# Optimization experiments

Hardware: AMD Instinct MI355X
Metric: run time of the kernel (lower is better)

## Reference

```python
import jax, jax.numpy as jnp
import numpy as np

N, E, D, ED, L = 40000, 640000, 128, 16, 3  # nodes, edges, emb_dim, edge_dim, num_layer
BN_EPS = 1e-5


def setup_inputs() -> dict:
    key = jax.random.key(0)
    ks = jax.random.split(key, 20)
    s = 0.05
    inp = {
        "x": jax.random.normal(ks[0], (N, D), jnp.float32),
        "edge_attr": jax.random.normal(ks[1], (E, ED), jnp.float32),
        # node encoder Linear(input_dim, emb_dim)
        "node_W": jax.random.normal(ks[2], (D, D), jnp.float32) * s,
        "node_b": jnp.zeros((D,), jnp.float32),
        # per-layer params (leading dim L)
        "edge_W": jax.random.normal(ks[3], (L, ED, D), jnp.float32) * s,
        "edge_b": jnp.zeros((L, D), jnp.float32),
        "attn_W": jax.random.normal(ks[4], (L, 2 * D, 1), jnp.float32) * s,
        "attn_b": jnp.zeros((L, 1), jnp.float32),
        "eps": jnp.zeros((L,), jnp.float32),
        "W1": jax.random.normal(ks[5], (L, D, 2 * D), jnp.float32) * s,
        "b1": jnp.zeros((L, 2 * D), jnp.float32),
        "bn1_g": jnp.ones((L, 2 * D), jnp.float32),
        "bn1_b": jnp.zeros((L, 2 * D), jnp.float32),
        "W2": jax.random.normal(ks[6], (L, 2 * D, D), jnp.float32) * s,
        "b2": jnp.zeros((L, D), jnp.float32),
        "bn_g": jnp.ones((L, D), jnp.float32),
        "bn_b": jnp.zeros((L, D), jnp.float32),
        "edge_index": jax.random.randint(ks[7], (2, E), 0, N, jnp.int32),
    }
    return inp


def _bn_eval(h, g, b):
    # BatchNorm1d in eval with running_mean=0, running_var=1
    return g * h * (1.0 / np.sqrt(1.0 + BN_EPS)) + b


def reference(x, edge_attr, node_W, node_b, edge_W, edge_b, attn_W, attn_b,
              eps, W1, b1, bn1_g, bn1_b, W2, b2, bn_g, bn_b, edge_index):
    src, dst = edge_index[0], edge_index[1]
    h = x @ node_W + node_b  # node_encoder, [N, D]
    for l in range(L):
        e = edge_attr @ edge_W[l] + edge_b[l]       # [E, D] edge embedding
        xj = h[src]                                  # [E, D] source gather
        xi = h[dst]                                  # [E, D] target gather
        a = jax.nn.sigmoid(jnp.concatenate([xi, xj], axis=-1) @ attn_W[l] + attn_b[l])  # [E,1]
        msg = jax.nn.relu(xj * a + e)                # fused per-edge message
        agg = jax.ops.segment_sum(msg, dst, num_segments=N)  # scatter-add aggregate
        z = (1.0 + eps[l]) * h + agg
        # GIN mlp: Linear -> BN(eval) -> ReLU -> Linear
        z = _bn_eval(z @ W1[l] + b1[l], bn1_g[l], bn1_b[l])
        z = jax.nn.relu(z)
        z = z @ W2[l] + b2[l]
        # outer BatchNorm(eval); dropout = identity in eval; JK='last', no residual
        z = _bn_eval(z, bn_g[l], bn_b[l])
        if l < L - 1:
            z = jax.nn.relu(z)
        h = z
    return h
```

## Files before the change

kernel.cpp:

```cpp
#include <hip/hip_runtime.h>
#include <math.h>

#define NN 40000
#define EE 640000
#define DD 128
#define EDD 16
#define LL 3
#define TEB 64

__device__ __constant__ float kBnInv = 0.9999950000374997f;

typedef __bf16 bf16x8 __attribute__((ext_vector_type(8)));
typedef float  f32x16 __attribute__((ext_vector_type(16)));
typedef float  f32x4  __attribute__((ext_vector_type(4)));
typedef float  f32x2  __attribute__((ext_vector_type(2)));

__device__ __forceinline__ unsigned pack_bf2(float a, float b) {
    unsigned ua = __float_as_uint(a), ub = __float_as_uint(b);
    ua = (ua + 0x7fffu + ((ua >> 16) & 1u)) >> 16;
    ub = (ub + 0x7fffu + ((ub >> 16) & 1u)) & 0xffff0000u;
    return ua | ub;
}
__device__ __forceinline__ unsigned short bf16r(float x) {
    unsigned u = __float_as_uint(x);
    u = (u + 0x7fffu + ((u >> 16) & 1u)) >> 16;
    return (unsigned short)u;
}

__global__ __launch_bounds__(256) void node_enc_kernel(
    const float* __restrict__ x, const float* __restrict__ W,
    const float* __restrict__ b,
    const float* __restrict__ aW, const float* __restrict__ eps_p,
    float* __restrict__ h, unsigned* __restrict__ hb,
    float* __restrict__ pi, float* __restrict__ pj, float* __restrict__ z)
{
    __shared__ float xs[32][DD];
    const int t = threadIdx.x;
    const long rowbase = (long)blockIdx.x * 32;

    const float4* x4 = (const float4*)(x + rowbase * DD);
    float4* xs4 = (float4*)&xs[0][0];
#pragma unroll
    for (int i = 0; i < 4; i++) xs4[t + i * 256] = x4[t + i * 256];
    __syncthreads();

    const int c  = (t & 31) * 4;
    const int r0 = (t >> 5) * 4;

    float acc[4][4] = {};
    for (int k4 = 0; k4 < DD; k4 += 4) {
        float4 xr[4];
#pragma unroll
        for (int i = 0; i < 4; i++) xr[i] = *(const float4*)&xs[r0 + i][k4];
#pragma unroll
        for (int kk = 0; kk < 4; kk++) {
            const float4 w = *(const float4*)(W + (k4 + kk) * DD + c);
#pragma unroll
            for (int i = 0; i < 4; i++) {
                const float xv = ((const float*)&xr[i])[kk];
                acc[i][0] = fmaf(xv, w.x, acc[i][0]);
                acc[i][1] = fmaf(xv, w.y, acc[i][1]);
                acc[i][2] = fmaf(xv, w.z, acc[i][2]);
                acc[i][3] = fmaf(xv, w.w, acc[i][3]);
            }
        }
    }
    const float4 bv  = *(const float4*)(b + c);
    const float4 awi = *(const float4*)(aW + c);
    const float4 awj = *(const float4*)(aW + DD + c);
    const float ep = 1.0f + eps_p[0];

    float pa[4], pb[4];
#pragma unroll
    for (int i = 0; i < 4; i++) {
        const long row = rowbase + r0 + i;
        float4 ov = { acc[i][0] + bv.x, acc[i][1] + bv.y,
                      acc[i][2] + bv.z, acc[i][3] + bv.w };
        *(float4*)(h + row * DD + c) = ov;
        uint2 pv = { pack_bf2(ov.x, ov.y), pack_bf2(ov.z, ov.w) };
        *(uint2*)(hb + row * 64 + (c >> 1)) = pv;
        float4 zv = { ep * ov.x, ep * ov.y, ep * ov.z, ep * ov.w };
        *(float4*)(z + row * DD + c) = zv;
        pa[i] = ov.x * awi.x + ov.y * awi.y + ov.z * awi.z + ov.w * awi.w;
        pb[i] = ov.x * awj.x + ov.y * awj.y + ov.z * awj.z + ov.w * awj.w;
    }
#pragma unroll
    for (int off = 1; off < 32; off <<= 1) {
#pragma unroll
        for (int i = 0; i < 4; i++) {
            pa[i] += __shfl_xor(pa[i], off, 64);
            pb[i] += __shfl_xor(pb[i], off, 64);
        }
    }
    if ((t & 31) == 0) {
#pragma unroll
        for (int i = 0; i < 4; i++) {
            pi[rowbase + r0 + i] = pa[i];
            pj[rowbase + r0 + i] = pb[i];
        }
    }
}

__global__ __launch_bounds__(256) void wcast_kernel(
    const float* __restrict__ W1, const float* __restrict__ W2,
    const float* __restrict__ eW,
    unsigned short* __restrict__ w1t, unsigned short* __restrict__ w2t,
    unsigned short* __restrict__ ewt)
{
    const int idx = blockIdx.x * 256 + threadIdx.x;
    const int l = idx >> 15, r = idx & 32767;
    {   const int n = r >> 7, k = r & 127;
        w1t[idx] = bf16r(W1[(l << 15) + (k << 8) + n]);
    }
    {   const int n = r >> 8, k = r & 255;
        w2t[idx] = bf16r(W2[(l << 15) + (k << 7) + n]);
    }
    if (idx < LL * 2048) {
        const int le = idx >> 11, re = idx & 2047;
        const int n = re >> 4, k = re & 15;
        ewt[idx] = bf16r(eW[(le << 11) + (k << 7) + n]);
    }
}

__global__ __launch_bounds__(256) void hist_kernel(
    const int* __restrict__ edge_index, int* __restrict__ counts)
{
    const int i = blockIdx.x * 256 + threadIdx.x;
    atomicAdd(&counts[edge_index[EE + i]], 1);
}

__global__ __launch_bounds__(256) void scan1_kernel(
    const int* __restrict__ counts, int* __restrict__ scanned,
    int* __restrict__ partials)
{
    __shared__ int sdata[256];
    const int t = threadIdx.x;
    const int base = blockIdx.x * 1024 + t * 4;
    int v[4]; int sum = 0;
#pragma unroll
    for (int i = 0; i < 4; i++) {
        const int idx = base + i;
        v[i] = (idx < NN) ? counts[idx] : 0;
        sum += v[i];
    }
    sdata[t] = sum;
    __syncthreads();
    for (int off = 1; off < 256; off <<= 1) {
        int x = (t >= off) ? sdata[t - off] : 0;
        __syncthreads();
        sdata[t] += x;
        __syncthreads();
    }
    int run = sdata[t] - sum;
#pragma unroll
    for (int i = 0; i < 4; i++) {
        const int idx = base + i;
        if (idx < NN) scanned[idx] = run;
        run += v[i];
    }
    if (t == 255) partials[blockIdx.x] = sdata[255];
}

__global__ void scan2_kernel(int* __restrict__ partials)
{
    if (threadIdx.x == 0) {
        int run = 0;
        for (int i = 0; i < 40; i++) { int v = partials[i]; partials[i] = run; run += v; }
    }
}

__global__ __launch_bounds__(256) void scan3_kernel(
    const int* __restrict__ scanned, const int* __restrict__ partials,
    int* __restrict__ offsets, int* __restrict__ cursor)
{
    const int idx = blockIdx.x * 256 + threadIdx.x;
    if (idx < NN) {
        const int off = scanned[idx] + partials[idx >> 10];
        offsets[idx] = off;
        cursor[idx]  = off;
    }
}

__global__ __launch_bounds__(256) void scatter_kernel(
    const int* __restrict__ edge_index, const float* __restrict__ edge_attr,
    int* __restrict__ cursor,
    int* __restrict__ srcs_p, int* __restrict__ dstd_p,
    unsigned* __restrict__ ea_b)
{
    const int i = blockIdx.x * 256 + threadIdx.x;
    const int src = edge_index[i];
    const int dst = edge_index[EE + i];
    const int pos = atomicAdd(&cursor[dst], 1);
    srcs_p[pos] = src << 6;
    dstd_p[pos] = dst << 7;

    const float4* sp = (const float4*)(edge_attr + (long)i * EDD);
    const float4 s0 = sp[0], s1 = sp[1], s2 = sp[2], s3 = sp[3];
    uint4 o0 = { pack_bf2(s0.x, s0.y), pack_bf2(s0.z, s0.w),
                 pack_bf2(s1.x, s1.y), pack_bf2(s1.z, s1.w) };
    uint4 o1 = { pack_bf2(s2.x, s2.y), pack_bf2(s2.z, s2.w),
                 pack_bf2(s3.x, s3.y), pack_bf2(s3.z, s3.w) };
    *(uint4*)(ea_b + (long)pos * 8)     = o0;
    *(uint4*)(ea_b + (long)pos * 8 + 4) = o1;
}

__global__ __launch_bounds__(256) void edge_msg_kernel(
    const unsigned* __restrict__ hb, const unsigned* __restrict__ ea_b,
    const float* __restrict__ pi, const float* __restrict__ pj,
    const int* __restrict__ srcs_p, const int* __restrict__ dstd_p,
    const float* __restrict__ ab_p,
    const unsigned short* __restrict__ eWt, const float* __restrict__ eb,
    float* __restrict__ z)
{
    __shared__ __align__(16) unsigned short sh_eb[TEB * DD];
    __shared__ int   sh_src[TEB];
    __shared__ int   sh_dst[TEB];
    __shared__ float sh_a[TEB];

    const int t = threadIdx.x;
    const int wid = t >> 6, lane = t & 63;
    const long e0 = (long)blockIdx.x * TEB;

    if (t < TEB) {
        const int ss = srcs_p[e0 + t];
        const int dd = dstd_p[e0 + t];
        sh_src[t] = ss;
        sh_dst[t] = dd;
        const float s = pi[dd >> 7] + pj[ss >> 6] + ab_p[0];
        sh_a[t] = 1.0f / (1.0f + expf(-s));
    }

    const int l31 = lane & 31, half = lane >> 5;
    const int mt = wid & 1, nt0 = wid >> 1;
    const bf16x8 afr  = *(const bf16x8*)(ea_b + (e0 + mt * 32 + l31) * 8 + half * 4);
    const bf16x8 bfr0 = *(const bf16x8*)(eWt + (nt0 * 32 + l31) * 16 + half * 8);
    const bf16x8 bfr1 = *(const bf16x8*)(eWt + ((nt0 + 2) * 32 + l31) * 16 + half * 8);

    __syncthreads();

    const int base = wid * 16;
    unsigned u[16];
#pragma unroll
    for (int j = 0; j < 16; j++)
        u[j] = hb[sh_src[base + j] + lane];

    {
        f32x16 a0 = {0.0f,0.0f,0.0f,0.0f, 0.0f,0.0f,0.0f,0.0f,
                     0.0f,0.0f,0.0f,0.0f, 0.0f,0.0f,0.0f,0.0f};
        f32x16 a1 = a0;
        a0 = __builtin_amdgcn_mfma_f32_32x32x16_bf16(afr, bfr0, a0, 0, 0, 0);
        a1 = __builtin_amdgcn_mfma_f32_32x32x16_bf16(afr, bfr1, a1, 0, 0, 0);
        const float eb0 = eb[nt0 * 32 + l31];
        const float eb1 = eb[(nt0 + 2) * 32 + l31];
        const int rb = mt * 32 + 4 * half;
        const int cA = nt0 * 32 + l31;
        const int cB = (nt0 + 2) * 32 + l31;
#pragma unroll
        for (int r = 0; r < 16; r++) {
            const int row = rb + (r & 3) + 8 * (r >> 2);
            sh_eb[row * DD + cA] = bf16r(a0[r] + eb0);
            sh_eb[row * DD + cB] = bf16r(a1[r] + eb1);
        }
    }
    __syncthreads();

    const int c0 = lane * 2;
    const f32x2 zero2 = { 0.0f, 0.0f };
    f32x2 acc = zero2;
    int cur = sh_dst[base];

#pragma unroll
    for (int j = 0; j < 16; j++) {
        const int dd = sh_dst[base + j];
        if (dd != cur) {
            atomicAdd(&z[cur + c0],     acc[0]);
            atomicAdd(&z[cur + c0 + 1], acc[1]);
            acc = zero2; cur = dd;
        }
        const float a = sh_a[base + j];
        const unsigned ue = *(const unsigned*)&sh_eb[(base + j) * DD + c0];
        const f32x2 ev = { __uint_as_float(ue << 16),
                           __uint_as_float(ue & 0xffff0000u) };
        const f32x2 xj = { __uint_as_float(u[j] << 16),
                           __uint_as_float(u[j] & 0xffff0000u) };
        const f32x2 av = { a, a };
        f32x2 m = __builtin_elementwise_fma(xj, av, ev);
        m = __builtin_elementwise_max(m, zero2);
        acc += m;
    }
    atomicAdd(&z[cur + c0],     acc[0]);
    atomicAdd(&z[cur + c0 + 1], acc[1]);
}

__global__ __launch_bounds__(256) void mlp_mfma_kernel(
    const float* __restrict__ zin,
    const unsigned short* __restrict__ w1t, const unsigned short* __restrict__ w2t,
    const float* __restrict__ b1, const float* __restrict__ g1, const float* __restrict__ bb1,
    const float* __restrict__ b2, const float* __restrict__ g2, const float* __restrict__ bb2,
    const float* __restrict__ aWn, const float* __restrict__ epsn_p,
    float* __restrict__ out, unsigned* __restrict__ hb,
    float* __restrict__ pi, float* __restrict__ pj, float* __restrict__ z,
    const int do_relu)
{
    __shared__ __align__(16) unsigned short zsb[64][136];
    __shared__ __align__(16) unsigned short usb[64][264];
    __shared__ float sh_pi[64], sh_pj[64];
    const int t = threadIdx.x;
    const int wid = t >> 6, lane = t & 63;
    const long rowbase = (long)blockIdx.x * 64;

    if (t < 64) { sh_pi[t] = 0.0f; sh_pj[t] = 0.0f; }

    {
        const float4* z4 = (const float4*)(zin + rowbase * DD);
#pragma unroll
        for (int i = 0; i < 8; i++) {
            const int idx = t + i * 256;
            const float4 v = z4[idx];
            const int row = idx >> 5;
            const int c4  = (idx & 31) * 4;
            uint2 pv = { pack_bf2(v.x, v.y), pack_bf2(v.z, v.w) };
            *(uint2*)&zsb[row][c4] = pv;
        }
    }
    __syncthreads();

    const int mrow  = lane & 15;
    const int quad  = lane >> 4;
    const f32x4 vzero = {0.0f, 0.0f, 0.0f, 0.0f};

    {
        const int nt0 = wid * 4;
        bf16x8 bf[4][4];
#pragma unroll
        for (int j = 0; j < 4; j++) {
            const unsigned short* wp = w1t + ((nt0 + j) * 16 + mrow) * 128 + quad * 8;
#pragma unroll
            for (int ks = 0; ks < 4; ks++)
                bf[j][ks] = *(const bf16x8*)(wp + ks * 32);
        }
        float gg[4], bi[4], bt[4];
#pragma unroll
        for (int j = 0; j < 4; j++) {
            const int c = (nt0 + j) * 16 + mrow;
            gg[j] = g1[c]; bi[j] = b1[c]; bt[j] = bb1[c];
        }
#pragma unroll
        for (int rt = 0; rt < 4; rt++) {
            bf16x8 af[4];
#pragma unroll
            for (int ks = 0; ks < 4; ks++)
                af[ks] = *(const bf16x8*)&zsb[rt * 16 + mrow][ks * 32 + quad * 8];
            f32x4 acc[4];
#pragma unroll
            for (int j = 0; j < 4; j++) acc[j] = vzero;
#pragma unroll
            for (int j = 0; j < 4; j++)
#pragma unroll
                for (int ks = 0; ks < 4; ks++)
                    acc[j] = __builtin_amdgcn_mfma_f32_16x16x32_bf16(af[ks], bf[j][ks], acc[j], 0, 0, 0);
#pragma unroll
            for (int j = 0; j < 4; j++) {
                const int c = (nt0 + j) * 16 + mrow;
#pragma unroll
                for (int r = 0; r < 4; r++) {
                    const int row = rt * 16 + quad * 4 + r;
                    const float u = fmaxf(fmaf(gg[j] * (acc[j][r] + bi[j]), kBnInv, bt[j]), 0.0f);
                    const float up = __shfl_xor(u, 1, 64);
                    if ((mrow & 1) == 0)
                        *(unsigned*)&usb[row][c] = pack_bf2(u, up);
                }
            }
        }
    }
    __syncthreads();

    {
        const int nt0 = wid * 2;
        bf16x8 bf[2][8];
#pragma unroll
        for (int j = 0; j < 2; j++) {
            const unsigned short* wp = w2t + ((nt0 + j) * 16 + mrow) * 256 + quad * 8;
#pragma unroll
            for (int ks = 0; ks < 8; ks++)
                bf[j][ks] = *(const bf16x8*)(wp + ks * 32);
        }
        float gg[2], bi[2], bt[2], awi[2], awj[2];
#pragma unroll
        for (int j = 0; j < 2; j++) {
            const int c = (nt0 + j) * 16 + mrow;
            gg[j] = g2[c]; bi[j] = b2[c]; bt[j] = bb2[c];
            awi[j] = aWn[c]; awj[j] = aWn[DD + c];
        }
        const float epn = do_relu ? (1.0f + epsn_p[0]) : 0.0f;

#pragma unroll
        for (int rt = 0; rt < 4; rt++) {
            bf16x8 af[8];
#pragma unroll
            for (int ks = 0; ks < 8; ks++)
                af[ks] = *(const bf16x8*)&usb[rt * 16 + mrow][ks * 32 + quad * 8];
            f32x4 acc[2];
            acc[0] = vzero; acc[1] = vzero;
#pragma unroll
            for (int j = 0; j < 2; j++)
#pragma unroll
                for (int ks = 0; ks < 8; ks++)
                    acc[j] = __builtin_amdgcn_mfma_f32_16x16x32_bf16(af[ks], bf[j][ks], acc[j], 0, 0, 0);

            float si[4] = {0, 0, 0, 0}, sj[4] = {0, 0, 0, 0};
#pragma unroll
            for (int j = 0; j < 2; j++) {
                const int c = (nt0 + j) * 16 + mrow;
#pragma unroll
                for (int r = 0; r < 4; r++) {
                    const long row = rowbase + rt * 16 + quad * 4 + r;
                    float v = fmaf(gg[j] * (acc[j][r] + bi[j]), kBnInv, bt[j]);
                    if (do_relu) {
                        v = fmaxf(v, 0.0f);
                        z[row * DD + c] = epn * v;
                        si[r] = fmaf(v, awi[j], si[r]);
                        sj[r] = fmaf(v, awj[j], sj[r]);
                    }
                    out[row * DD + c] = v;
                    const float vp = __shfl_xor(v, 1, 64);
                    if ((mrow & 1) == 0)
                        hb[row * 64 + (c >> 1)] = pack_bf2(v, vp);
                }
            }
            if (do_relu) {
#pragma unroll
                for (int off = 1; off < 16; off <<= 1) {
#pragma unroll
                    for (int r = 0; r < 4; r++) {
                        si[r] += __shfl_xor(si[r], off, 64);
                        sj[r] += __shfl_xor(sj[r], off, 64);
                    }
                }
                if (mrow == 0) {
#pragma unroll
                    for (int r = 0; r < 4; r++) {
                        atomicAdd(&sh_pi[rt * 16 + quad * 4 + r], si[r]);
                        atomicAdd(&sh_pj[rt * 16 + quad * 4 + r], sj[r]);
                    }
                }
            }
        }
    }
    if (do_relu) {
        __syncthreads();
        if (t < 64) {
            pi[rowbase + t] = sh_pi[t];
            pj[rowbase + t] = sh_pj[t];
        }
    }
}

extern "C" void kernel_launch(void* const* d_in, const int* in_sizes, int n_in,
                              void* d_out, int out_size, void* d_ws, size_t ws_size,
                              hipStream_t stream)
{
    const float* x         = (const float*)d_in[0];
    const float* edge_attr = (const float*)d_in[1];
    const float* node_W    = (const float*)d_in[2];
    const float* node_b    = (const float*)d_in[3];
    const float* edge_W    = (const float*)d_in[4];
    const float* edge_b    = (const float*)d_in[5];
    const float* attn_W    = (const float*)d_in[6];
    const float* attn_b    = (const float*)d_in[7];
    const float* eps       = (const float*)d_in[8];
    const float* W1        = (const float*)d_in[9];
    const float* b1        = (const float*)d_in[10];
    const float* bn1_g     = (const float*)d_in[11];
    const float* bn1_b     = (const float*)d_in[12];
    const float* W2        = (const float*)d_in[13];
    const float* b2        = (const float*)d_in[14];
    const float* bn_g      = (const float*)d_in[15];
    const float* bn_b      = (const float*)d_in[16];
    const int*   edge_index= (const int*)d_in[17];

    float* h    = (float*)d_ws;
    float* z    = h + (size_t)NN * DD;
    float* pi   = z + (size_t)NN * DD;
    float* pj   = pi + NN;
    unsigned* ea_b = (unsigned*)(pj + NN);
    unsigned* hbuf = ea_b + (size_t)EE * 8;
    unsigned short* w1t = (unsigned short*)(hbuf + (size_t)NN * 64);
    unsigned short* w2t = w1t + (size_t)LL * 32768;
    unsigned short* ewt = w2t + (size_t)LL * 32768;
    int* counts  = (int*)(ewt + (size_t)LL * 2048);
    int* offsets = counts + NN;
    int* cursor  = offsets + NN;
    int* scanned = cursor + NN;
    int* partials= scanned + 40960;
    int* srcs_p  = partials + 64;
    int* dstd_p  = srcs_p + EE;
    float* out = (float*)d_out;

    node_enc_kernel<<<NN / 32, 256, 0, stream>>>(
        x, node_W, node_b, attn_W, eps, h, hbuf, pi, pj, z);
    wcast_kernel<<<LL * 128, 256, 0, stream>>>(W1, W2, edge_W, w1t, w2t, ewt);

    hipMemsetAsync(counts, 0, NN * sizeof(int), stream);
    hist_kernel<<<EE / 256, 256, 0, stream>>>(edge_index, counts);
    scan1_kernel<<<40, 256, 0, stream>>>(counts, scanned, partials);
    scan2_kernel<<<1, 64, 0, stream>>>(partials);
    scan3_kernel<<<(NN + 255) / 256, 256, 0, stream>>>(scanned, partials, offsets, cursor);
    scatter_kernel<<<EE / 256, 256, 0, stream>>>(
        edge_index, edge_attr, cursor, srcs_p, dstd_p, ea_b);

    for (int l = 0; l < LL; l++) {
        const int ln = (l + 1 < LL) ? (l + 1) : l;
        edge_msg_kernel<<<EE / TEB, 256, 0, stream>>>(
            hbuf, ea_b, pi, pj, srcs_p, dstd_p, attn_b + l,
            ewt + (size_t)l * 2048, edge_b + (size_t)l * DD, z);
        mlp_mfma_kernel<<<NN / 64, 256, 0, stream>>>(
            z,
            w1t + (size_t)l * 32768, w2t + (size_t)l * 32768,
            b1 + (size_t)l * 2 * DD, bn1_g + (size_t)l * 2 * DD, bn1_b + (size_t)l * 2 * DD,
            b2 + (size_t)l * DD, bn_g + (size_t)l * DD, bn_b + (size_t)l * DD,
            attn_W + (size_t)ln * 2 * DD, eps + ln,
            (l == LL - 1) ? out : h, hbuf, pi, pj, z, (l < LL - 1) ? 1 : 0);
    }
}
```

Measured before the change: 531.2 us.

## Assign destination-node ranges to blocks and aggregate edge messages in LDS

The edge message kernel is re-partitioned so each block owns 32 consecutive destination nodes and walks their CSR-sorted edge range, accumulating messages in shared memory instead of issuing global float atomics. The block then writes z = (1+eps)*h + agg directly, so the node encoder and MLP kernels no longer pre-write z. This removes the global atomic traffic and the extra z stores. In exchange it adds load imbalance across blocks with uneven degree, extra syncthreads per 64-edge tile, and shared-memory atomics.

```diff
diff --git a/kernel.cpp b/kernel.cpp
--- a/kernel.cpp
+++ b/kernel.cpp
@@ -7,6 +7,7 @@
 #define EDD 16
 #define LL 3
 #define TEB 64
+#define NPB 32
 
 __device__ __constant__ float kBnInv = 0.9999950000374997f;
 
@@ -30,9 +31,9 @@
 __global__ __launch_bounds__(256) void node_enc_kernel(
     const float* __restrict__ x, const float* __restrict__ W,
     const float* __restrict__ b,
-    const float* __restrict__ aW, const float* __restrict__ eps_p,
+    const float* __restrict__ aW,
     float* __restrict__ h, unsigned* __restrict__ hb,
-    float* __restrict__ pi, float* __restrict__ pj, float* __restrict__ z)
+    float* __restrict__ pi, float* __restrict__ pj)
 {
     __shared__ float xs[32][DD];
     const int t = threadIdx.x;
@@ -68,7 +69,6 @@
     const float4 bv  = *(const float4*)(b + c);
     const float4 awi = *(const float4*)(aW + c);
     const float4 awj = *(const float4*)(aW + DD + c);
-    const float ep = 1.0f + eps_p[0];
 
     float pa[4], pb[4];
 #pragma unroll
@@ -79,8 +79,6 @@
         *(float4*)(h + row * DD + c) = ov;
         uint2 pv = { pack_bf2(ov.x, ov.y), pack_bf2(ov.z, ov.w) };
         *(uint2*)(hb + row * 64 + (c >> 1)) = pv;
-        float4 zv = { ep * ov.x, ep * ov.y, ep * ov.z, ep * ov.w };
-        *(float4*)(z + row * DD + c) = zv;
         pa[i] = ov.x * awi.x + ov.y * awi.y + ov.z * awi.z + ov.w * awi.w;
         pb[i] = ov.x * awj.x + ov.y * awj.y + ov.z * awj.z + ov.w * awj.w;
     }
@@ -208,88 +206,128 @@
     const unsigned* __restrict__ hb, const unsigned* __restrict__ ea_b,
     const float* __restrict__ pi, const float* __restrict__ pj,
     const int* __restrict__ srcs_p, const int* __restrict__ dstd_p,
+    const int* __restrict__ offsets,
     const float* __restrict__ ab_p,
     const unsigned short* __restrict__ eWt, const float* __restrict__ eb,
+    const float* __restrict__ h, const float* __restrict__ eps_p,
     float* __restrict__ z)
 {
     __shared__ __align__(16) unsigned short sh_eb[TEB * DD];
+    __shared__ __align__(16) float sh_agg[NPB * DD];
     __shared__ int   sh_src[TEB];
-    __shared__ int   sh_dst[TEB];
+    __shared__ int   sh_ldst[TEB];
     __shared__ float sh_a[TEB];
+    __shared__ float sh_piL[NPB];
 
     const int t = threadIdx.x;
     const int wid = t >> 6, lane = t & 63;
-    const long e0 = (long)blockIdx.x * TEB;
-
-    if (t < TEB) {
-        const int ss = srcs_p[e0 + t];
-        const int dd = dstd_p[e0 + t];
-        sh_src[t] = ss;
-        sh_dst[t] = dd;
-        const float s = pi[dd >> 7] + pj[ss >> 6] + ab_p[0];
-        sh_a[t] = 1.0f / (1.0f + expf(-s));
-    }
+    const int n0 = blockIdx.x * NPB;
+    const int ebeg = offsets[n0];
+    const int eend = (n0 + NPB < NN) ? offsets[n0 + NPB] : EE;
+
+    {
+        f32x4* a4 = (f32x4*)sh_agg;
+        const f32x4 z4v = {0.0f, 0.0f, 0.0f, 0.0f};
+#pragma unroll
+        for (int i = 0; i < 4; i++) a4[t + i * 256] = z4v;
+    }
+    if (t < NPB) sh_piL[t] = pi[n0 + t];
 
     const int l31 = lane & 31, half = lane >> 5;
     const int mt = wid & 1, nt0 = wid >> 1;
-    const bf16x8 afr  = *(const bf16x8*)(ea_b + (e0 + mt * 32 + l31) * 8 + half * 4);
     const bf16x8 bfr0 = *(const bf16x8*)(eWt + (nt0 * 32 + l31) * 16 + half * 8);
     const bf16x8 bfr1 = *(const bf16x8*)(eWt + ((nt0 + 2) * 32 + l31) * 16 + half * 8);
-
-    __syncthreads();
-
-    const int base = wid * 16;
-    unsigned u[16];
-#pragma unroll
-    for (int j = 0; j < 16; j++)
-        u[j] = hb[sh_src[base + j] + lane];
-
-    {
-        f32x16 a0 = {0.0f,0.0f,0.0f,0.0f, 0.0f,0.0f,0.0f,0.0f,
-                     0.0f,0.0f,0.0f,0.0f, 0.0f,0.0f,0.0f,0.0f};
-        f32x16 a1 = a0;
-        a0 = __builtin_amdgcn_mfma_f32_32x32x16_bf16(afr, bfr0, a0, 0, 0, 0);
-        a1 = __builtin_amdgcn_mfma_f32_32x32x16_bf16(afr, bfr1, a1, 0, 0, 0);
-        const float eb0 = eb[nt0 * 32 + l31];
-        const float eb1 = eb[(nt0 + 2) * 32 + l31];
-        const int rb = mt * 32 + 4 * half;
-        const int cA = nt0 * 32 + l31;
-        const int cB = (nt0 + 2) * 32 + l31;
-#pragma unroll
-        for (int r = 0; r < 16; r++) {
-            const int row = rb + (r & 3) + 8 * (r >> 2);
-            sh_eb[row * DD + cA] = bf16r(a0[r] + eb0);
-            sh_eb[row * DD + cB] = bf16r(a1[r] + eb1);
-        }
-    }
-    __syncthreads();
-
+    const float eb0 = eb[nt0 * 32 + l31];
+    const float eb1 = eb[(nt0 + 2) * 32 + l31];
+    const float ab0 = ab_p[0];
+    const int rb = mt * 32 + 4 * half;
+    const int cA = nt0 * 32 + l31;
+    const int cB = (nt0 + 2) * 32 + l31;
+    const int baseL = wid * 16;
     const int c0 = lane * 2;
     const f32x2 zero2 = { 0.0f, 0.0f };
-    f32x2 acc = zero2;
-    int cur = sh_dst[base];
-
-#pragma unroll
-    for (int j = 0; j < 16; j++) {
-        const int dd = sh_dst[base + j];
-        if (dd != cur) {
-            atomicAdd(&z[cur + c0],     acc[0]);
-            atomicAdd(&z[cur + c0 + 1], acc[1]);
-            acc = zero2; cur = dd;
-        }
-        const float a = sh_a[base + j];
-        const unsigned ue = *(const unsigned*)&sh_eb[(base + j) * DD + c0];
-        const f32x2 ev = { __uint_as_float(ue << 16),
-                           __uint_as_float(ue & 0xffff0000u) };
-        const f32x2 xj = { __uint_as_float(u[j] << 16),
-                           __uint_as_float(u[j] & 0xffff0000u) };
-        const f32x2 av = { a, a };
-        f32x2 m = __builtin_elementwise_fma(xj, av, ev);
-        m = __builtin_elementwise_max(m, zero2);
-        acc += m;
-    }
-    atomicAdd(&z[cur + c0],     acc[0]);
-    atomicAdd(&z[cur + c0 + 1], acc[1]);
+
+    __syncthreads();
+
+    for (int tb = ebeg; tb < eend; tb += TEB) {
+        if (t < TEB) {
+            const int e = tb + t;
+            int ss = 0, ld = 0; float a = 0.0f;
+            if (e < eend) {
+                ss = srcs_p[e];
+                ld = (dstd_p[e] >> 7) - n0;
+                const float s = sh_piL[ld] + pj[ss >> 6] + ab0;
+                a = 1.0f / (1.0f + expf(-s));
+            }
+            sh_src[t] = ss; sh_ldst[t] = ld; sh_a[t] = a;
+        }
+        __syncthreads();
+
+        unsigned u[16];
+#pragma unroll
+        for (int j = 0; j < 16; j++)
+            u[j] = hb[sh_src[baseL + j] + lane];
+
+        {
+            const bf16x8 afr = *(const bf16x8*)(ea_b + ((long)(tb + mt * 32 + l31)) * 8 + half * 4);
+            f32x16 a0 = {0.0f,0.0f,0.0f,0.0f, 0.0f,0.0f,0.0f,0.0f,
+                         0.0f,0.0f,0.0f,0.0f, 0.0f,0.0f,0.0f,0.0f};
+            f32x16 a1 = a0;
+            a0 = __builtin_amdgcn_mfma_f32_32x32x16_bf16(afr, bfr0, a0, 0, 0, 0);
+            a1 = __builtin_amdgcn_mfma_f32_32x32x16_bf16(afr, bfr1, a1, 0, 0, 0);
+#pragma unroll
+            for (int r = 0; r < 16; r++) {
+                const int row = rb + (r & 3) + 8 * (r >> 2);
+                sh_eb[row * DD + cA] = bf16r(a0[r] + eb0);
+                sh_eb[row * DD + cB] = bf16r(a1[r] + eb1);
+            }
+        }
+        __syncthreads();
+
+        int nv = eend - (tb + baseL);
+        nv = nv > 16 ? 16 : nv;
+        if (nv > 0) {
+            f32x2 acc = zero2;
+            int cur = sh_ldst[baseL];
+#pragma unroll
+            for (int j = 0; j < 16; j++) {
+                if (j >= nv) break;
+                const int dd = sh_ldst[baseL + j];
+                if (dd != cur) {
+                    atomicAdd(&sh_agg[cur * DD + c0],     acc[0]);
+                    atomicAdd(&sh_agg[cur * DD + c0 + 1], acc[1]);
+                    acc = zero2; cur = dd;
+                }
+                const float a = sh_a[baseL + j];
+                const unsigned ue = *(const unsigned*)&sh_eb[(baseL + j) * DD + c0];
+                const f32x2 ev = { __uint_as_float(ue << 16),
+                                   __uint_as_float(ue & 0xffff0000u) };
+                const f32x2 xj = { __uint_as_float(u[j] << 16),
+                                   __uint_as_float(u[j] & 0xffff0000u) };
+                const f32x2 av = { a, a };
+                f32x2 m = __builtin_elementwise_fma(xj, av, ev);
+                m = __builtin_elementwise_max(m, zero2);
+                acc += m;
+            }
+            atomicAdd(&sh_agg[cur * DD + c0],     acc[0]);
+            atomicAdd(&sh_agg[cur * DD + c0 + 1], acc[1]);
+        }
+        __syncthreads();
+    }
+
+    const float ep = 1.0f + eps_p[0];
+    const float4* h4 = (const float4*)(h + (long)n0 * DD);
+    float4* z4 = (float4*)(z + (long)n0 * DD);
+    const f32x4* a4 = (const f32x4*)sh_agg;
+#pragma unroll
+    for (int i = 0; i < 4; i++) {
+        const int idx = t + i * 256;
+        const float4 hv = h4[idx];
+        const f32x4 av = a4[idx];
+        float4 zv = { fmaf(ep, hv.x, av[0]), fmaf(ep, hv.y, av[1]),
+                      fmaf(ep, hv.z, av[2]), fmaf(ep, hv.w, av[3]) };
+        z4[idx] = zv;
+    }
 }
 
 __global__ __launch_bounds__(256) void mlp_mfma_kernel(
@@ -297,9 +335,9 @@
     const unsigned short* __restrict__ w1t, const unsigned short* __restrict__ w2t,
     const float* __restrict__ b1, const float* __restrict__ g1, const float* __restrict__ bb1,
     const float* __restrict__ b2, const float* __restrict__ g2, const float* __restrict__ bb2,
-    const float* __restrict__ aWn, const float* __restrict__ epsn_p,
+    const float* __restrict__ aWn,
     float* __restrict__ out, unsigned* __restrict__ hb,
-    float* __restrict__ pi, float* __restrict__ pj, float* __restrict__ z,
+    float* __restrict__ pi, float* __restrict__ pj,
     const int do_relu)
 {
     __shared__ __align__(16) unsigned short zsb[64][136];
@@ -392,7 +430,6 @@
             gg[j] = g2[c]; bi[j] = b2[c]; bt[j] = bb2[c];
             awi[j] = aWn[c]; awj[j] = aWn[DD + c];
         }
-        const float epn = do_relu ? (1.0f + epsn_p[0]) : 0.0f;
 
 #pragma unroll
         for (int rt = 0; rt < 4; rt++) {
@@ -418,7 +455,6 @@
                     float v = fmaf(gg[j] * (acc[j][r] + bi[j]), kBnInv, bt[j]);
                     if (do_relu) {
                         v = fmaxf(v, 0.0f);
-                        z[row * DD + c] = epn * v;
                         si[r] = fmaf(v, awi[j], si[r]);
                         sj[r] = fmaf(v, awj[j], sj[r]);
                     }
@@ -498,7 +534,7 @@
     float* out = (float*)d_out;
 
     node_enc_kernel<<<NN / 32, 256, 0, stream>>>(
-        x, node_W, node_b, attn_W, eps, h, hbuf, pi, pj, z);
+        x, node_W, node_b, attn_W, h, hbuf, pi, pj);
     wcast_kernel<<<LL * 128, 256, 0, stream>>>(W1, W2, edge_W, w1t, w2t, ewt);
 
     hipMemsetAsync(counts, 0, NN * sizeof(int), stream);
@@ -511,15 +547,16 @@
 
     for (int l = 0; l < LL; l++) {
         const int ln = (l + 1 < LL) ? (l + 1) : l;
-        edge_msg_kernel<<<EE / TEB, 256, 0, stream>>>(
-            hbuf, ea_b, pi, pj, srcs_p, dstd_p, attn_b + l,
-            ewt + (size_t)l * 2048, edge_b + (size_t)l * DD, z);
+        edge_msg_kernel<<<NN / NPB, 256, 0, stream>>>(
+            hbuf, ea_b, pi, pj, srcs_p, dstd_p, offsets, attn_b + l,
+            ewt + (size_t)l * 2048, edge_b + (size_t)l * DD,
+            h, eps + l, z);
         mlp_mfma_kernel<<<NN / 64, 256, 0, stream>>>(
             z,
             w1t + (size_t)l * 32768, w2t + (size_t)l * 32768,
             b1 + (size_t)l * 2 * DD, bn1_g + (size_t)l * 2 * DD, bn1_b + (size_t)l * 2 * DD,
             b2 + (size_t)l * DD, bn_g + (size_t)l * DD, bn_b + (size_t)l * DD,
-            attn_W + (size_t)ln * 2 * DD, eps + ln,
-            (l == LL - 1) ? out : h, hbuf, pi, pj, z, (l < LL - 1) ? 1 : 0);
-    }
-}
+            attn_W + (size_t)ln * 2 * DD,
+            (l == LL - 1) ? out : h, hbuf, pi, pj, (l < LL - 1) ? 1 : 0);
+    }
+}
```

New measurement: 652.5 us. 22.8% more time.
